# Kernel optimization log

Hardware: AMD Instinct MI355X
Metric: run time of the kernel (lower is better)

The kernel has to match this reference:

```python
import jax, jax.numpy as jnp
import numpy as np

B, T, D, H = 32, 1024, 256, 256
STDV = 1.0 / np.sqrt(H)


def _uni(key, shape):
    return jax.random.uniform(key, shape, jnp.float32, -STDV, STDV)


def setup_inputs() -> dict:
    key = jax.random.key(0)
    ks = jax.random.split(key, 16)
    inp = {"x": jax.random.normal(ks[0], (B, T, D), jnp.float32)}
    names = ["l1_W", "l1_U", "l1_b", "l1_Wb", "l1_Ub", "l1_bb",
             "l2_Wx", "l2_Wh", "l2_U", "l2_b", "l2_Wxb", "l2_Whb", "l2_Ub", "l2_bb"]
    shapes = {"b": (4, H)}
    for i, n in enumerate(names):
        suffix = n.split("_")[1]
        if suffix.startswith("b"):
            shp = (4, H)
        elif suffix.startswith("Wx") or (n in ("l1_W", "l1_Wb")):
            shp = (4, D, H)
        else:
            shp = (4, H, H)
        inp[n] = _uni(ks[i + 1], shp)
    return inp


def _bilstm_dir(x, W, U, b):
    # x: [B,T,Din]; W: [4,Din,H]; U: [4,H,H]; b: [4,H]
    xp = jnp.einsum('btd,gdh->tbgh', x, W) + b  # precompute input projections
    h0 = jnp.zeros((x.shape[0], H), x.dtype)

    def step(carry, xpt):
        h, c = carry
        gates = jax.nn.sigmoid(xpt + jnp.einsum('bh,gho->bgo', h, U))
        i, f, g, o = gates[:, 0], gates[:, 1], gates[:, 2], gates[:, 3]
        c = f + c + i * g          # NOTE: additive, as in source
        h = o + jnp.tanh(c)        # NOTE: additive, as in source
        return (h, c), h

    (hT, _), hs = jax.lax.scan(step, (h0, h0), xp)
    return hs, hT  # hs: [T,B,H]


def _bvlstm_dir(x, hp, Wx, Wh, U, b):
    # x: [B,T,D]; hp: [B,T,H]. Bug in source: all gates use u_i (U[0]) and b_i (b[0]).
    xp = jnp.einsum('btd,gdh->tbgh', x, Wx) + jnp.einsum('bth,gho->tbgo', hp, Wh)
    h0 = jnp.zeros((x.shape[0], H), x.dtype)

    def step(carry, xpt):
        h, c = carry
        hu = h @ U[0] + b[0]  # shared recurrent term across all 4 gates (source bug)
        gates = jax.nn.sigmoid(xpt + hu[:, None, :])
        i, f, g, o = gates[:, 0], gates[:, 1], gates[:, 2], gates[:, 3]
        c = f + c + i * g
        h = o + jnp.tanh(c)
        return (h, c), h

    (hT, _), hs = jax.lax.scan(step, (h0, h0), xp)
    return hs, hT


def _bilstm(x, W, U, b, Wb, Ub, bb):
    hs_f, h_f = _bilstm_dir(x, W, U, b)
    hs_b, h_b = _bilstm_dir(x[:, ::-1], Wb, Ub, bb)
    y_net = jnp.concatenate([jnp.transpose(hs_f, (1, 0, 2)),
                             jnp.transpose(hs_b[::-1], (1, 0, 2))], axis=2)
    y_t = jnp.concatenate([h_f, h_b], axis=1)
    return y_t, y_net


def _bvlstm(x, h_prev, Wx, Wh, U, b, Wxb, Whb, Ub, bb):
    hp_f = h_prev[:, :, :H]
    hp_b = h_prev[:, :, H:2 * H]
    hs_f, h_f = _bvlstm_dir(x, hp_f, Wx, Wh, U, b)
    hs_b, h_b = _bvlstm_dir(x[:, ::-1], hp_b[:, ::-1], Wxb, Whb, Ub, bb)
    y_net = jnp.concatenate([jnp.transpose(hs_f, (1, 0, 2)),
                             jnp.transpose(hs_b[::-1], (1, 0, 2))], axis=2)
    y_t = jnp.concatenate([h_f, h_b], axis=1)
    return y_t, y_net


def reference(x, l1_W, l1_U, l1_b, l1_Wb, l1_Ub, l1_bb,
              l2_Wx, l2_Wh, l2_U, l2_b, l2_Wxb, l2_Whb, l2_Ub, l2_bb):
    _, y_net1 = _bilstm(x, l1_W, l1_U, l1_b, l1_Wb, l1_Ub, l1_bb)
    y_t2, y_net2 = _bvlstm(x, y_net1, l2_Wx, l2_Wh, l2_U, l2_b,
                           l2_Wxb, l2_Whb, l2_Ub, l2_bb)
    return y_t2, y_net2
```

## Files before the change

### kernel.cpp

```cpp
#include <hip/hip_runtime.h>
#include <hip/hip_bf16.h>
#include <stdint.h>


typedef unsigned short u16;
typedef unsigned int   u32;
typedef __attribute__((ext_vector_type(8))) short s8v;
typedef __attribute__((ext_vector_type(4))) float f4v;
typedef __attribute__((ext_vector_type(4))) u32   u32x4;

__device__ __forceinline__ f4v mfma16(s8v a, s8v b, f4v c) {
  return __builtin_amdgcn_mfma_f32_16x16x32_bf16(a, b, c, 0, 0, 0);
}

__device__ __forceinline__ u16 f2bf(float f) {
  u32 u = __float_as_uint(f);
  return (u16)((u + 0x7FFFu + ((u >> 16) & 1u)) >> 16);
}
__device__ __forceinline__ float bf2f(u16 h) {
  return __uint_as_float(((u32)h) << 16);
}
__device__ __forceinline__ float sigm(float x) {
  return __builtin_amdgcn_rcpf(1.0f + __expf(-x));
}
__device__ __forceinline__ float tanh_f(float x) {
  return 1.0f - 2.0f * __builtin_amdgcn_rcpf(__expf(2.0f * x) + 1.0f);
}


__global__ void k_wconv(const float* __restrict__ src, u16* __restrict__ dst) {
  int o = blockIdx.x * 256 + threadIdx.x;
  int j = o & 7, col = (o >> 3) & 1023, kg = o >> 13;
  int g = col >> 8, h = col & 255, k = (kg << 3) + j;
  dst[o] = f2bf(src[((g << 8) + k) * 256 + h]);
}

__global__ void k_uconv1(const float* __restrict__ src, u16* __restrict__ dst) {
  int o = blockIdx.x * 256 + threadIdx.x;
  int j = o & 7, l = (o >> 3) & 63, fi = (o >> 9) & 31, hcx = (o >> 14) & 1, wg = o >> 15;
  int g = fi >> 3, s = fi & 7;
  int k = s * 32 + ((l >> 4) << 3) + j;
  int h = wg * 32 + hcx * 16 + (l & 15);
  dst[o] = f2bf(src[((g << 8) + k) * 256 + h]);
}

__global__ void k_uconv2(const float* __restrict__ src, u16* __restrict__ dst) {
  int o = blockIdx.x * 256 + threadIdx.x;
  int j = o & 7, l = (o >> 3) & 63, s = (o >> 9) & 7, nt = (o >> 12) & 1, wg = o >> 13;
  int k = s * 32 + ((l >> 4) << 3) + j;
  int h = wg * 32 + nt * 16 + (l & 15);
  dst[o] = f2bf(src[k * 256 + h]);
}

__global__ void k_canary(float* __restrict__ out, int n) {
  int i = blockIdx.x * 256 + threadIdx.x;
  if (i < n) out[i] = 1.0e9f;
}

__global__ __launch_bounds__(256) void k_gemm(
    const float* __restrict__ X, const u16* __restrict__ A1,
    const u16* __restrict__ Bg, const float* __restrict__ bias,
    u16* __restrict__ C, int K, int rev)
{
  __shared__ __align__(16) u16 At[128 * 32];
  __shared__ __align__(16) u16 Bt[4 * 128 * 8];
  const int tid = threadIdx.x, l = tid & 63, w = tid >> 6;
  const int wm = w >> 1, wn = w & 1;
  const int m0 = blockIdx.y * 128, n0 = blockIdx.x * 128;
  f4v z = {0.f, 0.f, 0.f, 0.f};
  f4v acc[4][4];
  #pragma unroll
  for (int a = 0; a < 4; ++a)
    #pragma unroll
    for (int b = 0; b < 4; ++b) acc[a][b] = z;

  const int nk = K >> 5;
  for (int ki = 0; ki < nk; ++ki) {
    #pragma unroll
    for (int i = 0; i < 2; ++i) {
      int id = tid + (i << 8);
      int row = id >> 2, kc = id & 3;
      int ks = (ki << 5) + (kc << 3);
      int gm = m0 + row;
      if (ks < 256) {
        int tt = gm >> 5, bb = gm & 31;
        int tsrc = rev ? (1023 - tt) : tt;
        const float4* s = (const float4*)(X + ((size_t)bb * 1024 + tsrc) * 256 + ks);
        float4 f0 = s[0], f1 = s[1];
        alignas(16) u16 tmp[8];
        tmp[0] = f2bf(f0.x); tmp[1] = f2bf(f0.y); tmp[2] = f2bf(f0.z); tmp[3] = f2bf(f0.w);
        tmp[4] = f2bf(f1.x); tmp[5] = f2bf(f1.y); tmp[6] = f2bf(f1.z); tmp[7] = f2bf(f1.w);
        *(uint4*)&At[id << 3] = *(const uint4*)tmp;
      } else {
        const u16* s = A1 + (size_t)gm * 256 + (ks - 256);
        *(uint4*)&At[id << 3] = *(const uint4*)s;
      }
      int kg = id >> 7, n = id & 127;
      const u16* s2 = Bg + (((size_t)(ki * 4 + kg) * 1024) + n0 + n) * 8;
      *(uint4*)&Bt[id << 3] = *(const uint4*)s2;
    }
    __syncthreads();
    s8v af[4], bf[4];
    #pragma unroll
    for (int mt = 0; mt < 4; ++mt)
      af[mt] = *(const s8v*)&At[((wm * 64 + mt * 16 + (l & 15)) * 32) + ((l >> 4) << 3)];
    #pragma unroll
    for (int nt = 0; nt < 4; ++nt)
      bf[nt] = *(const s8v*)&Bt[(((l >> 4) * 128) + wn * 64 + nt * 16 + (l & 15)) << 3];
    #pragma unroll
    for (int mt = 0; mt < 4; ++mt)
      #pragma unroll
      for (int nt = 0; nt < 4; ++nt)
        acc[mt][nt] = mfma16(af[mt], bf[nt], acc[mt][nt]);
    __syncthreads();
  }

  float bv[4];
  #pragma unroll
  for (int nt = 0; nt < 4; ++nt)
    bv[nt] = bias ? bias[n0 + wn * 64 + nt * 16 + (l & 15)] : 0.f;
  #pragma unroll
  for (int mt = 0; mt < 4; ++mt)
    #pragma unroll
    for (int nt = 0; nt < 4; ++nt)
      #pragma unroll
      for (int rr = 0; rr < 4; ++rr) {
        int row = m0 + wm * 64 + mt * 16 + ((l >> 4) << 2) + rr;
        int col = n0 + wn * 64 + nt * 16 + (l & 15);
        C[(size_t)row * 1024 + col] = f2bf(acc[mt][nt][rr] + bv[nt]);
      }
}


__device__ __forceinline__ void ldxp16(const u16* __restrict__ xp, int t,
                                       int rowbase, int hc, u16* q) {
  const u16* p = xp + ((size_t)t << 15);
  #pragma unroll
  for (int g = 0; g < 4; ++g)
    #pragma unroll
    for (int rr = 0; rr < 4; ++rr)
      q[g * 4 + rr] = p[(rowbase + rr) * 1024 + g * 256 + hc];
}

__device__ __forceinline__ void ld_h64(const u32* base, u32x4* r) {
  asm volatile(
    "global_load_dwordx4 %0, %16, off sc0 sc1\n\t"
    "global_load_dwordx4 %1, %16, off offset:16 sc0 sc1\n\t"
    "global_load_dwordx4 %2, %16, off offset:128 sc0 sc1\n\t"
    "global_load_dwordx4 %3, %16, off offset:144 sc0 sc1\n\t"
    "global_load_dwordx4 %4, %16, off offset:256 sc0 sc1\n\t"
    "global_load_dwordx4 %5, %16, off offset:272 sc0 sc1\n\t"
    "global_load_dwordx4 %6, %16, off offset:384 sc0 sc1\n\t"
    "global_load_dwordx4 %7, %16, off offset:400 sc0 sc1\n\t"
    "global_load_dwordx4 %8, %16, off offset:512 sc0 sc1\n\t"
    "global_load_dwordx4 %9, %16, off offset:528 sc0 sc1\n\t"
    "global_load_dwordx4 %10, %16, off offset:640 sc0 sc1\n\t"
    "global_load_dwordx4 %11, %16, off offset:656 sc0 sc1\n\t"
    "global_load_dwordx4 %12, %16, off offset:768 sc0 sc1\n\t"
    "global_load_dwordx4 %13, %16, off offset:784 sc0 sc1\n\t"
    "global_load_dwordx4 %14, %16, off offset:896 sc0 sc1\n\t"
    "global_load_dwordx4 %15, %16, off offset:912 sc0 sc1\n\t"
    "s_waitcnt vmcnt(0)"
    : "=&v"(r[0]), "=&v"(r[1]), "=&v"(r[2]), "=&v"(r[3]),
      "=&v"(r[4]), "=&v"(r[5]), "=&v"(r[6]), "=&v"(r[7]),
      "=&v"(r[8]), "=&v"(r[9]), "=&v"(r[10]), "=&v"(r[11]),
      "=&v"(r[12]), "=&v"(r[13]), "=&v"(r[14]), "=&v"(r[15])
    : "v"(base)
    : "memory");
}

__device__ __forceinline__ bool frags_from_tagged(const u32x4* r, u32 tag, s8v* af) {
  u32 bad = 0;
  #pragma unroll
  for (int s = 0; s < 8; ++s) {
    u32x4 a = r[2 * s], b = r[2 * s + 1];
    bad |= (a.x ^ tag) & 0xffffu; bad |= (a.y ^ tag) & 0xffffu;
    bad |= (a.z ^ tag) & 0xffffu; bad |= (a.w ^ tag) & 0xffffu;
    bad |= (b.x ^ tag) & 0xffffu; bad |= (b.y ^ tag) & 0xffffu;
    bad |= (b.z ^ tag) & 0xffffu; bad |= (b.w ^ tag) & 0xffffu;
    union { u32 d[4]; s8v v; } pk;
    pk.d[0] = (a.x >> 16) | (a.y & 0xffff0000u);
    pk.d[1] = (a.z >> 16) | (a.w & 0xffff0000u);
    pk.d[2] = (b.x >> 16) | (b.y & 0xffff0000u);
    pk.d[3] = (b.z >> 16) | (b.w & 0xffff0000u);
    af[s] = pk.v;
  }
  return !__any(bad != 0);
}

__device__ __forceinline__ void ld_h_frags(const u32* hr, u32 tag, s8v* af) {
  #pragma unroll 1
  for (int rtry = 0; ; ++rtry) {
    u32x4 r[16];
    ld_h64(hr, r);
    if (frags_from_tagged(r, tag, af)) return;
    if (rtry > (1 << 20)) {
      union { u32 d[4]; s8v v; } nn;
      nn.d[0] = nn.d[1] = nn.d[2] = nn.d[3] = 0x7FC07FC0u;
      #pragma unroll
      for (int s = 0; s < 8; ++s) af[s] = nn.v;
      return;
    }
  }
}

__device__ __forceinline__ void st_tagged(u32* p, u32 v) {
  __hip_atomic_store(p, v, __ATOMIC_RELAXED, __HIP_MEMORY_SCOPE_AGENT);
}

__global__ __launch_bounds__(256, 1) void k_scan1(
    const u16* __restrict__ xp_f, const u16* __restrict__ xp_b,
    const u16* __restrict__ Uf_f, const u16* __restrict__ Uf_b,
    u16* __restrict__ hs_f, u16* __restrict__ hs_b,
    u32* hbuf)
{
  const int bid = blockIdx.x;
  const int dir = bid >> 3, wg = bid & 7;
  const int tid = threadIdx.x, l = tid & 63, wv = tid >> 6;
  const int mt = wv >> 1, hcx = wv & 1;
  const u16* xp = dir ? xp_b : xp_f;
  const u16* Uf = dir ? Uf_b : Uf_f;
  u16* hs = dir ? hs_b : hs_f;
  u32* hb = hbuf + dir * 16384;

  const int hc = wg * 32 + hcx * 16 + (l & 15);
  const int rowbase = mt * 16 + ((l >> 4) << 2);
  const int arow = (mt * 16 + (l & 15)) * 256;
  const int kcol = (l >> 4) << 3;

  s8v uf[32];
  #pragma unroll
  for (int fi = 0; fi < 32; ++fi)
    uf[fi] = *(const s8v*)(Uf + ((((wg * 2 + hcx) * 32 + fi) * 64 + l) << 3));

  float c[4] = {0.f, 0.f, 0.f, 0.f};
  u16 xq[16];
  ldxp16(xp, 0, rowbase, hc, xq);

  #pragma unroll 1
  for (int t = 0; t < 1024; ++t) {
    u16 xc[16];
    #pragma unroll
    for (int i = 0; i < 16; ++i) xc[i] = xq[i];
    if (t < 1023) ldxp16(xp, t + 1, rowbase, hc, xq);

    f4v zz = {0.f, 0.f, 0.f, 0.f};
    f4v acc[4];
    #pragma unroll
    for (int g = 0; g < 4; ++g) acc[g] = zz;

    if (t > 0) {
      const u32* hr = hb + ((t & 1) << 13) + arow + kcol;
      s8v af[8];
      ld_h_frags(hr, (u32)t, af);
      #pragma unroll
      for (int s = 0; s < 8; ++s)
        #pragma unroll
        for (int g = 0; g < 4; ++g)
          acc[g] = mfma16(af[s], uf[g * 8 + s], acc[g]);
    }

    u32* hw = hb + (((t + 1) & 1) << 13);
    const u32 wtag = (u32)(t + 1);
    #pragma unroll
    for (int rr = 0; rr < 4; ++rr) {
      const int b = rowbase + rr;
      float si = sigm(bf2f(xc[0 * 4 + rr]) + acc[0][rr]);
      float sf = sigm(bf2f(xc[1 * 4 + rr]) + acc[1][rr]);
      float sg = sigm(bf2f(xc[2 * 4 + rr]) + acc[2][rr]);
      float so = sigm(bf2f(xc[3 * 4 + rr]) + acc[3][rr]);
      c[rr] = sf + c[rr] + si * sg;
      float h = so + tanh_f(c[rr]);
      u16 hv = f2bf(h);
      st_tagged(hw + b * 256 + hc, ((u32)hv << 16) | wtag);
      hs[((t << 5) + b) * 256 + hc] = hv;
    }
  }
}

__global__ __launch_bounds__(256, 1) void k_scan2(
    const u16* __restrict__ xp_f, const u16* __restrict__ xp_b,
    const u16* __restrict__ Uf_f, const u16* __restrict__ Uf_b,
    const float* __restrict__ b2_f, const float* __restrict__ b2_b,
    float* __restrict__ out,
    u32* hbuf)
{
  const int bid = blockIdx.x;
  const int dir = bid >> 3, wg = bid & 7;
  const int tid = threadIdx.x, l = tid & 63, wv = tid >> 6;
  const int mt = wv >> 1, nt = wv & 1;
  const u16* xp = dir ? xp_b : xp_f;
  const u16* Uf = dir ? Uf_b : Uf_f;
  const float* b2 = dir ? b2_b : b2_f;
  u32* hb = hbuf + dir * 16384;

  const int hc = wg * 32 + nt * 16 + (l & 15);
  const int rowbase = mt * 16 + ((l >> 4) << 2);
  const int arow = (mt * 16 + (l & 15)) * 256;
  const int kcol = (l >> 4) << 3;
  const float bv = b2[hc];
  const int jj = (dir ? 256 : 0) + hc;

  s8v uf[8];
  #pragma unroll
  for (int s = 0; s < 8; ++s)
    uf[s] = *(const s8v*)(Uf + ((((wg * 2 + nt) * 8 + s) * 64 + l) << 3));

  float c[4] = {0.f, 0.f, 0.f, 0.f};
  u16 xq[16];
  ldxp16(xp, 0, rowbase, hc, xq);

  #pragma unroll 1
  for (int t = 0; t < 1024; ++t) {
    u16 xc[16];
    #pragma unroll
    for (int i = 0; i < 16; ++i) xc[i] = xq[i];
    if (t < 1023) ldxp16(xp, t + 1, rowbase, hc, xq);

    f4v acc = {0.f, 0.f, 0.f, 0.f};
    if (t > 0) {
      const u32* hr = hb + ((t & 1) << 13) + arow + kcol;
      s8v af[8];
      ld_h_frags(hr, (u32)t, af);
      #pragma unroll
      for (int s = 0; s < 8; ++s)
        acc = mfma16(af[s], uf[s], acc);
    }

    u32* hw = hb + (((t + 1) & 1) << 13);
    const u32 wtag = (u32)(t + 1);
    const int tout = dir ? (1023 - t) : t;
    #pragma unroll
    for (int rr = 0; rr < 4; ++rr) {
      const int b = rowbase + rr;
      float hu = acc[rr] + bv;
      float si = sigm(bf2f(xc[0 * 4 + rr]) + hu);
      float sf = sigm(bf2f(xc[1 * 4 + rr]) + hu);
      float sg = sigm(bf2f(xc[2 * 4 + rr]) + hu);
      float so = sigm(bf2f(xc[3 * 4 + rr]) + hu);
      c[rr] = sf + c[rr] + si * sg;
      float h = so + tanh_f(c[rr]);
      st_tagged(hw + b * 256 + hc, ((u32)f2bf(h) << 16) | wtag);
      out[16384 + ((size_t)b * 1024 + tout) * 512 + jj] = h;
      if (t == 1023) out[b * 512 + jj] = h;
    }
  }
}

extern "C" void kernel_launch(void* const* d_in, const int* in_sizes, int n_in,
                              void* d_out, int out_size, void* d_ws, size_t ws_size,
                              hipStream_t stream)
{
  const float* x      = (const float*)d_in[0];
  const float* l1_W   = (const float*)d_in[1];
  const float* l1_U   = (const float*)d_in[2];
  const float* l1_b   = (const float*)d_in[3];
  const float* l1_Wb  = (const float*)d_in[4];
  const float* l1_Ub  = (const float*)d_in[5];
  const float* l1_bb  = (const float*)d_in[6];
  const float* l2_Wx  = (const float*)d_in[7];
  const float* l2_Wh  = (const float*)d_in[8];
  const float* l2_U   = (const float*)d_in[9];
  const float* l2_b   = (const float*)d_in[10];
  const float* l2_Wxb = (const float*)d_in[11];
  const float* l2_Whb = (const float*)d_in[12];
  const float* l2_Ub  = (const float*)d_in[13];
  const float* l2_bb  = (const float*)d_in[14];

  char* p0 = (char*)d_ws;
  char* p = p0;
  auto alloc = [&](size_t bytes) {
    char* r = p; p += (bytes + 255) & ~(size_t)255; return r;
  };
  u16*   xpf   = (u16*)  alloc(33554432ull * 2);
  u16*   xpb   = (u16*)  alloc(33554432ull * 2);
  u16*   hs1f  = (u16*)  alloc(8388608ull * 2);
  u16*   hs1b  = (u16*)  alloc(8388608ull * 2);
  u16*   W1f   = (u16*)  alloc(262144ull * 2);
  u16*   W1b   = (u16*)  alloc(262144ull * 2);
  u16*   Wc2f  = (u16*)  alloc(524288ull * 2);
  u16*   Wc2b  = (u16*)  alloc(524288ull * 2);
  u16*   Uf1f  = (u16*)  alloc(262144ull * 2);
  u16*   Uf1b  = (u16*)  alloc(262144ull * 2);
  u16*   Uf2f  = (u16*)  alloc(65536ull * 2);
  u16*   Uf2b  = (u16*)  alloc(65536ull * 2);
  u32*   hbuf1 = (u32*)  alloc(32768ull * 4);
  u32*   hbuf2 = (u32*)  alloc(32768ull * 4);
  if ((size_t)(p - p0) > ws_size) {
    k_canary<<<(out_size + 255) / 256, 256, 0, stream>>>((float*)d_out, out_size);
    return;
  }

  k_wconv<<<1024, 256, 0, stream>>>(l1_W,   W1f);
  k_wconv<<<1024, 256, 0, stream>>>(l1_Wb,  W1b);
  k_wconv<<<1024, 256, 0, stream>>>(l2_Wx,  Wc2f);
  k_wconv<<<1024, 256, 0, stream>>>(l2_Wh,  Wc2f + 262144);
  k_wconv<<<1024, 256, 0, stream>>>(l2_Wxb, Wc2b);
  k_wconv<<<1024, 256, 0, stream>>>(l2_Whb, Wc2b + 262144);
  k_uconv1<<<1024, 256, 0, stream>>>(l1_U,  Uf1f);
  k_uconv1<<<1024, 256, 0, stream>>>(l1_Ub, Uf1b);
  k_uconv2<<<256, 256, 0, stream>>>(l2_U,  Uf2f);
  k_uconv2<<<256, 256, 0, stream>>>(l2_Ub, Uf2b);

  dim3 gg(8, 256);
  k_gemm<<<gg, 256, 0, stream>>>(x, nullptr, W1f, l1_b,  xpf, 256, 0);
  k_gemm<<<gg, 256, 0, stream>>>(x, nullptr, W1b, l1_bb, xpb, 256, 1);

  k_scan1<<<16, 256, 0, stream>>>(xpf, xpb, Uf1f, Uf1b, hs1f, hs1b, hbuf1);

  k_gemm<<<gg, 256, 0, stream>>>(x, hs1f, Wc2f, nullptr, xpf, 512, 0);
  k_gemm<<<gg, 256, 0, stream>>>(x, hs1b, Wc2b, nullptr, xpb, 512, 1);

  k_scan2<<<16, 256, 0, stream>>>(xpf, xpb, Uf2f, Uf2b, l2_b, l2_bb,
                                  (float*)d_out, hbuf2);
}
```

Before: 9.123 ms.

## Run layer-2 scan in one workgroup per direction with LDS hidden state

The layer-2 recurrent scan moves from 8 cooperating workgroups per direction, which exchanged the hidden state through tagged global memory, to a single 1024-thread workgroup per direction. The state is kept in double-buffered LDS and each step ends with __syncthreads. This removes the cross-workgroup global-memory handshake and its polling latency on every timestep. The cost is that the whole scan runs on only two CUs, each wave doing twice the MFMA and gate work, and the U weight layout is permuted to match.

```diff
diff --git a/kernel.cpp b/kernel.cpp
--- a/kernel.cpp
+++ b/kernel.cpp
@@ -46,9 +46,9 @@
 
 __global__ void k_uconv2(const float* __restrict__ src, u16* __restrict__ dst) {
   int o = blockIdx.x * 256 + threadIdx.x;
-  int j = o & 7, l = (o >> 3) & 63, s = (o >> 9) & 7, nt = (o >> 12) & 1, wg = o >> 13;
-  int k = s * 32 + ((l >> 4) << 3) + j;
-  int h = wg * 32 + nt * 16 + (l & 15);
+  int j = o & 7, l = (o >> 3) & 63, kk = (o >> 9) & 7, cg = o >> 12;
+  int k = kk * 32 + ((l >> 4) << 3) + j;
+  int h = cg * 16 + (l & 15);
   dst[o] = f2bf(src[k * 256 + h]);
 }
 
@@ -278,72 +278,96 @@
   }
 }
 
-__global__ __launch_bounds__(256, 1) void k_scan2(
+__global__ __launch_bounds__(1024, 1) void k_scan2(
     const u16* __restrict__ xp_f, const u16* __restrict__ xp_b,
     const u16* __restrict__ Uf_f, const u16* __restrict__ Uf_b,
     const float* __restrict__ b2_f, const float* __restrict__ b2_b,
-    float* __restrict__ out,
-    u32* hbuf)
+    float* __restrict__ out)
 {
-  const int bid = blockIdx.x;
-  const int dir = bid >> 3, wg = bid & 7;
+  __shared__ __align__(16) u16 hl[2][2][8][64][8];
+  const int dir = blockIdx.x;
   const int tid = threadIdx.x, l = tid & 63, wv = tid >> 6;
-  const int mt = wv >> 1, nt = wv & 1;
   const u16* xp = dir ? xp_b : xp_f;
   const u16* Uf = dir ? Uf_b : Uf_f;
   const float* b2 = dir ? b2_b : b2_f;
-  u32* hb = hbuf + dir * 16384;
-
-  const int hc = wg * 32 + nt * 16 + (l & 15);
-  const int rowbase = mt * 16 + ((l >> 4) << 2);
-  const int arow = (mt * 16 + (l & 15)) * 256;
-  const int kcol = (l >> 4) << 3;
-  const float bv = b2[hc];
-  const int jj = (dir ? 256 : 0) + hc;
+
+  const int col = wv * 16 + (l & 15);
+  const int rbase = (l >> 4) << 2;
+  const float bv = b2[col];
+  const int jj = (dir ? 256 : 0) + col;
+  const int kkw = col >> 5, lhw = (col >> 3) & 3, jw = col & 7;
 
   s8v uf[8];
   #pragma unroll
-  for (int s = 0; s < 8; ++s)
-    uf[s] = *(const s8v*)(Uf + ((((wg * 2 + nt) * 8 + s) * 64 + l) << 3));
-
-  float c[4] = {0.f, 0.f, 0.f, 0.f};
-  u16 xq[16];
-  ldxp16(xp, 0, rowbase, hc, xq);
+  for (int kk = 0; kk < 8; ++kk)
+    uf[kk] = *(const s8v*)(Uf + (((wv * 8 + kk) * 64 + l) << 3));
+
+  float c[2][4];
+  #pragma unroll
+  for (int s = 0; s < 2; ++s)
+    #pragma unroll
+    for (int rr = 0; rr < 4; ++rr) c[s][rr] = 0.f;
+
+  u16 xq[32], xc[32];
+  {
+    const u16* p = xp;
+    #pragma unroll
+    for (int s = 0; s < 2; ++s)
+      #pragma unroll
+      for (int rr = 0; rr < 4; ++rr)
+        #pragma unroll
+        for (int g = 0; g < 4; ++g)
+          xq[(s * 4 + rr) * 4 + g] = p[(s * 16 + rbase + rr) * 1024 + g * 256 + col];
+  }
 
   #pragma unroll 1
   for (int t = 0; t < 1024; ++t) {
-    u16 xc[16];
-    #pragma unroll
-    for (int i = 0; i < 16; ++i) xc[i] = xq[i];
-    if (t < 1023) ldxp16(xp, t + 1, rowbase, hc, xq);
-
-    f4v acc = {0.f, 0.f, 0.f, 0.f};
+    #pragma unroll
+    for (int i = 0; i < 32; ++i) xc[i] = xq[i];
+    if (t < 1023) {
+      const u16* p = xp + ((size_t)(t + 1) << 15);
+      #pragma unroll
+      for (int s = 0; s < 2; ++s)
+        #pragma unroll
+        for (int rr = 0; rr < 4; ++rr)
+          #pragma unroll
+          for (int g = 0; g < 4; ++g)
+            xq[(s * 4 + rr) * 4 + g] = p[(s * 16 + rbase + rr) * 1024 + g * 256 + col];
+    }
+
+    f4v zz = {0.f, 0.f, 0.f, 0.f};
+    f4v acc[2]; acc[0] = zz; acc[1] = zz;
     if (t > 0) {
-      const u32* hr = hb + ((t & 1) << 13) + arow + kcol;
-      s8v af[8];
-      ld_h_frags(hr, (u32)t, af);
-      #pragma unroll
-      for (int s = 0; s < 8; ++s)
-        acc = mfma16(af[s], uf[s], acc);
-    }
-
-    u32* hw = hb + (((t + 1) & 1) << 13);
-    const u32 wtag = (u32)(t + 1);
+      const int par = (t - 1) & 1;
+      #pragma unroll
+      for (int s = 0; s < 2; ++s)
+        #pragma unroll
+        for (int kk = 0; kk < 8; ++kk) {
+          s8v a = *(const s8v*)&hl[par][s][kk][l][0];
+          acc[s] = mfma16(a, uf[kk], acc[s]);
+        }
+    }
+
+    const int parw = t & 1;
     const int tout = dir ? (1023 - t) : t;
     #pragma unroll
-    for (int rr = 0; rr < 4; ++rr) {
-      const int b = rowbase + rr;
-      float hu = acc[rr] + bv;
-      float si = sigm(bf2f(xc[0 * 4 + rr]) + hu);
-      float sf = sigm(bf2f(xc[1 * 4 + rr]) + hu);
-      float sg = sigm(bf2f(xc[2 * 4 + rr]) + hu);
-      float so = sigm(bf2f(xc[3 * 4 + rr]) + hu);
-      c[rr] = sf + c[rr] + si * sg;
-      float h = so + tanh_f(c[rr]);
-      st_tagged(hw + b * 256 + hc, ((u32)f2bf(h) << 16) | wtag);
-      out[16384 + ((size_t)b * 1024 + tout) * 512 + jj] = h;
-      if (t == 1023) out[b * 512 + jj] = h;
-    }
+    for (int s = 0; s < 2; ++s)
+      #pragma unroll
+      for (int rr = 0; rr < 4; ++rr) {
+        const int b = s * 16 + rbase + rr;
+        float hu = acc[s][rr] + bv;
+        const int base = (s * 4 + rr) * 4;
+        float si = sigm(bf2f(xc[base + 0]) + hu);
+        float sf = sigm(bf2f(xc[base + 1]) + hu);
+        float sg = sigm(bf2f(xc[base + 2]) + hu);
+        float so = sigm(bf2f(xc[base + 3]) + hu);
+        c[s][rr] = sf + c[s][rr] + si * sg;
+        float h = so + tanh_f(c[s][rr]);
+        hl[parw][s][kkw][lhw * 16 + (rbase + rr)][jw] = f2bf(h);
+        out[16384 + ((size_t)b * 1024 + tout) * 512 + jj] = h;
+        if (t == 1023) out[b * 512 + jj] = h;
+      }
+    __syncthreads();
   }
 }
 
@@ -385,7 +409,6 @@
   u16*   Uf2f  = (u16*)  alloc(65536ull * 2);
   u16*   Uf2b  = (u16*)  alloc(65536ull * 2);
   u32*   hbuf1 = (u32*)  alloc(32768ull * 4);
-  u32*   hbuf2 = (u32*)  alloc(32768ull * 4);
   if ((size_t)(p - p0) > ws_size) {
     k_canary<<<(out_size + 255) / 256, 256, 0, stream>>>((float*)d_out, out_size);
     return;
@@ -411,6 +434,6 @@
   k_gemm<<<gg, 256, 0, stream>>>(x, hs1f, Wc2f, nullptr, xpf, 512, 0);
   k_gemm<<<gg, 256, 0, stream>>>(x, hs1b, Wc2b, nullptr, xpb, 512, 1);
 
-  k_scan2<<<16, 256, 0, stream>>>(xpf, xpb, Uf2f, Uf2b, l2_b, l2_bb,
-                                  (float*)d_out, hbuf2);
-}
+  k_scan2<<<2, 1024, 0, stream>>>(xpf, xpb, Uf2f, Uf2b, l2_b, l2_bb,
+                                  (float*)d_out);
+}
```

New measurement: 18.01 ms. 1.97x slower.
